# Kernel optimization log

Measured on AMD Instinct MI355X. Metric: run time of the kernel, lower is better.

## Reference

```python
import jax, jax.numpy as jnp
import numpy as np

SCALE, Z, X, Y = 4, 9, 9, 9
INV_SQRT_2PI = 1.0 / np.sqrt(2.0 * np.pi)


def setup_inputs() -> dict:
    key = jax.random.key(0)
    k1, = jax.random.split(key, 1)
    inp = jax.random.normal(k1, (1, 1, 128, 512, 512), dtype=jnp.float32)
    return {
        "inp": inp,
        "mu_z": jnp.asarray(0.0, dtype=jnp.float32),
        "sig_z": jnp.asarray(0.1, dtype=jnp.float32),
        "bet_xy": jnp.asarray(2.0, dtype=jnp.float32),
        "bet_z": jnp.asarray(1.5, dtype=jnp.float32),
    }


def _gen_alf(bet_xy, bet_z):
    # squared distances along each axis; torch's loop overwrites the wrap-around
    # write, so the net result for odd sizes is simply (arange - size//2)**2
    zd = ((jnp.arange(Z) - Z // 2) ** 2).astype(jnp.float32)[:, None, None]
    xd = ((jnp.arange(X) - X // 2) ** 2).astype(jnp.float32)[None, :, None]
    yd = ((jnp.arange(Y) - Y // 2) ** 2).astype(jnp.float32)[None, None, :]
    d_2 = zd / bet_z ** 2 + (xd + yd) / bet_xy ** 2  # (Z, X, Y)
    return jnp.exp(-d_2 / 2) * INV_SQRT_2PI


def reference(inp, mu_z, sig_z, bet_xy, bet_z):
    z0 = jnp.exp(mu_z + 0.5 * sig_z ** 2)
    rec = inp * z0  # (N, 1, D, H, W)
    alf = _gen_alf(bet_xy, bet_z)[None, None]  # (1, 1, Z, X, Y)
    pad_z = (Z - SCALE + 1) // 2
    rec = jax.lax.conv_general_dilated(
        rec, alf,
        window_strides=(SCALE, 1, 1),
        padding=[(pad_z, pad_z), (X // 2, X // 2), (Y // 2, Y // 2)],
        dimension_numbers=("NCDHW", "OIDHW", "NCDHW"),
    )  # (N, 1, D//SCALE, H, W)
    rec = (rec - rec.min()) / (rec.max() - rec.min())
    return rec
```

## Files before the change

kernel.cpp:

```cpp
#include <hip/hip_runtime.h>

#define D_IN  128
#define D_OUT 32
#define H     512
#define W     512
#define W4    128

__device__ __forceinline__ float gw(int k, float inv2) {
    float d = (float)(k - 4);
    return expf(-d * d * inv2);
}

__global__ void zconv_kernel(const float* __restrict__ inp, float* __restrict__ out,
                             const float* __restrict__ bet_z_p) {
    int tid = blockIdx.x * blockDim.x + threadIdx.x;
    int w4 = tid & (W4 - 1);
    int h  = (tid >> 7) & (H - 1);
    int d  = tid >> 16;
    float bz   = bet_z_p[0];
    float inv2 = 1.0f / (2.0f * bz * bz);
    const float4* in4 = (const float4*)inp;
    float4 acc = make_float4(0.f, 0.f, 0.f, 0.f);
    int base = h * W4 + w4;
#pragma unroll
    for (int k = 0; k < 9; ++k) {
        int din = 4 * d - 3 + k;
        if (din < 0 || din >= D_IN) continue;
        float wt = gw(k, inv2);
        float4 v = in4[din * (H * W4) + base];
        acc.x += v.x * wt; acc.y += v.y * wt; acc.z += v.z * wt; acc.w += v.w * wt;
    }
    ((float4*)out)[d * (H * W4) + base] = acc;
}

__global__ void hconv_kernel(const float* __restrict__ in, float* __restrict__ out,
                             const float* __restrict__ bet_xy_p) {
    int tid = blockIdx.x * blockDim.x + threadIdx.x;
    int w4 = tid & (W4 - 1);
    int h  = (tid >> 7) & (H - 1);
    int d  = tid >> 16;
    float b    = bet_xy_p[0];
    float inv2 = 1.0f / (2.0f * b * b);
    const float4* in4 = (const float4*)in;
    float4 acc = make_float4(0.f, 0.f, 0.f, 0.f);
#pragma unroll
    for (int k = 0; k < 9; ++k) {
        int hh = h - 4 + k;
        if (hh < 0 || hh >= H) continue;
        float wt = gw(k, inv2);
        float4 v = in4[(d * H + hh) * W4 + w4];
        acc.x += v.x * wt; acc.y += v.y * wt; acc.z += v.z * wt; acc.w += v.w * wt;
    }
    ((float4*)out)[(d * H + h) * W4 + w4] = acc;
}

__global__ void wconv_kernel(const float* __restrict__ in, float* __restrict__ out,
                             const float* __restrict__ bet_xy_p,
                             float* __restrict__ blkMin, float* __restrict__ blkMax) {
    int tid = blockIdx.x * blockDim.x + threadIdx.x;
    int w4 = tid & (W4 - 1);
    int h  = (tid >> 7) & (H - 1);
    int d  = tid >> 16;
    float b    = bet_xy_p[0];
    float inv2 = 1.0f / (2.0f * b * b);
    float wt[9];
#pragma unroll
    for (int k = 0; k < 9; ++k) wt[k] = gw(k, inv2);

    const float4* in4 = (const float4*)in;
    int row = (d * H + h) * W4;
    float4 z4 = make_float4(0.f, 0.f, 0.f, 0.f);
    float4 va = (w4 > 0)      ? in4[row + w4 - 1] : z4;
    float4 vb =                 in4[row + w4];
    float4 vc = (w4 < W4 - 1) ? in4[row + w4 + 1] : z4;
    float win[12] = {va.x, va.y, va.z, va.w,
                     vb.x, vb.y, vb.z, vb.w,
                     vc.x, vc.y, vc.z, vc.w};
    float4 o = make_float4(0.f, 0.f, 0.f, 0.f);
#pragma unroll
    for (int k = 0; k < 9; ++k) {
        o.x += win[k]     * wt[k];
        o.y += win[k + 1] * wt[k];
        o.z += win[k + 2] * wt[k];
        o.w += win[k + 3] * wt[k];
    }
    ((float4*)out)[row + w4] = o;

    float lmin = fminf(fminf(o.x, o.y), fminf(o.z, o.w));
    float lmax = fmaxf(fmaxf(o.x, o.y), fmaxf(o.z, o.w));
#pragma unroll
    for (int off = 32; off > 0; off >>= 1) {
        lmin = fminf(lmin, __shfl_down(lmin, off, 64));
        lmax = fmaxf(lmax, __shfl_down(lmax, off, 64));
    }
    __shared__ float smin[4], smax[4];
    int lane = threadIdx.x & 63, wv = threadIdx.x >> 6;
    if (lane == 0) { smin[wv] = lmin; smax[wv] = lmax; }
    __syncthreads();
    if (threadIdx.x == 0) {
        blkMin[blockIdx.x] = fminf(fminf(smin[0], smin[1]), fminf(smin[2], smin[3]));
        blkMax[blockIdx.x] = fmaxf(fmaxf(smax[0], smax[1]), fmaxf(smax[2], smax[3]));
    }
}

__global__ void reduce_kernel(const float* __restrict__ blkMin, const float* __restrict__ blkMax,
                              float* __restrict__ fin, int nblk) {
    float lmin =  3.402823466e38f;
    float lmax = -3.402823466e38f;
    for (int i = threadIdx.x; i < nblk; i += blockDim.x) {
        lmin = fminf(lmin, blkMin[i]);
        lmax = fmaxf(lmax, blkMax[i]);
    }
#pragma unroll
    for (int off = 32; off > 0; off >>= 1) {
        lmin = fminf(lmin, __shfl_down(lmin, off, 64));
        lmax = fmaxf(lmax, __shfl_down(lmax, off, 64));
    }
    __shared__ float smin[4], smax[4];
    int lane = threadIdx.x & 63, wv = threadIdx.x >> 6;
    if (lane == 0) { smin[wv] = lmin; smax[wv] = lmax; }
    __syncthreads();
    if (threadIdx.x == 0) {
        fin[0] = fminf(fminf(smin[0], smin[1]), fminf(smin[2], smin[3]));
        fin[1] = fmaxf(fmaxf(smax[0], smax[1]), fmaxf(smax[2], smax[3]));
    }
}

__global__ void norm_kernel(const float* __restrict__ in, float* __restrict__ out,
                            const float* __restrict__ fin) {
    int tid = blockIdx.x * blockDim.x + threadIdx.x;
    float mn  = fin[0];
    float inv = 1.0f / (fin[1] - mn);
    float4 v = ((const float4*)in)[tid];
    float4 o = make_float4((v.x - mn) * inv, (v.y - mn) * inv,
                           (v.z - mn) * inv, (v.w - mn) * inv);
    ((float4*)out)[tid] = o;
}

extern "C" void kernel_launch(void* const* d_in, const int* in_sizes, int n_in,
                              void* d_out, int out_size, void* d_ws, size_t ws_size,
                              hipStream_t stream) {
    const float* inp    = (const float*)d_in[0];
    const float* bet_xy = (const float*)d_in[3];
    const float* bet_z  = (const float*)d_in[4];
    float* out = (float*)d_out;

    char* ws = (char*)d_ws;
    float* fin    = (float*)ws;
    float* blkMin = (float*)(ws + 256);
    float* blkMax = (float*)(ws + 256 + 32768);
    float* bufA   = (float*)(ws + 256 + 65536);

    const int NTH  = D_OUT * H * W4;
    const int BLK  = 256;
    const int GRID = NTH / BLK;

    zconv_kernel<<<GRID, BLK, 0, stream>>>(inp, bufA, bet_z);
    hconv_kernel<<<GRID, BLK, 0, stream>>>(bufA, out, bet_xy);
    wconv_kernel<<<GRID, BLK, 0, stream>>>(out, bufA, bet_xy, blkMin, blkMax);
    reduce_kernel<<<1, BLK, 0, stream>>>(blkMin, blkMax, fin, GRID);
    norm_kernel<<<GRID, BLK, 0, stream>>>(bufA, out, fin);
}
```

Before: 275.0 us.

## Fuse z, h, w separable convolutions into one LDS-tiled kernel

Replaces the three separate z, h and w convolution kernels with a single kernel. Each block handles a 16-row strip of one output depth slice and keeps the z-convolved strip (with halo) and the h-convolved strip in shared memory. This removes two full intermediate round trips through global memory. In exchange it recomputes the z-conv for 8 halo rows per strip (24/16 of the input reads) and uses about 80KB of LDS per block, which limits occupancy.

```diff
diff --git a/kernel.cpp b/kernel.cpp
--- a/kernel.cpp
+++ b/kernel.cpp
@@ -5,101 +5,112 @@
 #define H     512
 #define W     512
 #define W4    128
+#define HB    16
+#define ZR    (HB + 8)
+#define NTHR  512
 
-__device__ __forceinline__ float gw(int k, float inv2) {
-    float d = (float)(k - 4);
-    return expf(-d * d * inv2);
-}
+__global__ __launch_bounds__(NTHR)
+void conv3d_fused(const float* __restrict__ inp, float* __restrict__ out,
+                  const float* __restrict__ bxy_p, const float* __restrict__ bz_p,
+                  float* __restrict__ blkMin, float* __restrict__ blkMax) {
+    __shared__ float zbuf[ZR * W];
+    __shared__ float hbuf[HB * W];
 
-__global__ void zconv_kernel(const float* __restrict__ inp, float* __restrict__ out,
-                             const float* __restrict__ bet_z_p) {
-    int tid = blockIdx.x * blockDim.x + threadIdx.x;
-    int w4 = tid & (W4 - 1);
-    int h  = (tid >> 7) & (H - 1);
-    int d  = tid >> 16;
-    float bz   = bet_z_p[0];
-    float inv2 = 1.0f / (2.0f * bz * bz);
-    const float4* in4 = (const float4*)inp;
-    float4 acc = make_float4(0.f, 0.f, 0.f, 0.f);
-    int base = h * W4 + w4;
+    const int d  = blockIdx.x >> 5;
+    const int h0 = (blockIdx.x & 31) * HB;
+
+    const float bz = bz_p[0], bx = bxy_p[0];
+    const float iz = 1.0f / (2.0f * bz * bz);
+    const float ix = 1.0f / (2.0f * bx * bx);
+    float wz[9], wx[9];
 #pragma unroll
     for (int k = 0; k < 9; ++k) {
-        int din = 4 * d - 3 + k;
-        if (din < 0 || din >= D_IN) continue;
-        float wt = gw(k, inv2);
-        float4 v = in4[din * (H * W4) + base];
-        acc.x += v.x * wt; acc.y += v.y * wt; acc.z += v.z * wt; acc.w += v.w * wt;
+        float dd = (float)(k - 4);
+        wz[k] = expf(-dd * dd * iz);
+        wx[k] = expf(-dd * dd * ix);
     }
-    ((float4*)out)[d * (H * W4) + base] = acc;
-}
 
-__global__ void hconv_kernel(const float* __restrict__ in, float* __restrict__ out,
-                             const float* __restrict__ bet_xy_p) {
-    int tid = blockIdx.x * blockDim.x + threadIdx.x;
-    int w4 = tid & (W4 - 1);
-    int h  = (tid >> 7) & (H - 1);
-    int d  = tid >> 16;
-    float b    = bet_xy_p[0];
-    float inv2 = 1.0f / (2.0f * b * b);
-    const float4* in4 = (const float4*)in;
-    float4 acc = make_float4(0.f, 0.f, 0.f, 0.f);
+    const float4* in4 = (const float4*)inp;
+    float4* z4 = (float4*)zbuf;
+    float4* h4 = (float4*)hbuf;
+
+    for (int t = threadIdx.x; t < ZR * W4; t += NTHR) {
+        int r  = t >> 7;
+        int c4 = t & (W4 - 1);
+        int h  = h0 - 4 + r;
+        float4 acc = make_float4(0.f, 0.f, 0.f, 0.f);
+        if ((unsigned)h < H) {
+            int base = h * W4 + c4;
 #pragma unroll
-    for (int k = 0; k < 9; ++k) {
-        int hh = h - 4 + k;
-        if (hh < 0 || hh >= H) continue;
-        float wt = gw(k, inv2);
-        float4 v = in4[(d * H + hh) * W4 + w4];
-        acc.x += v.x * wt; acc.y += v.y * wt; acc.z += v.z * wt; acc.w += v.w * wt;
+            for (int k = 0; k < 9; ++k) {
+                int din = 4 * d - 3 + k;
+                if ((unsigned)din < D_IN) {
+                    float4 v = in4[din * (H * W4) + base];
+                    acc.x += v.x * wz[k]; acc.y += v.y * wz[k];
+                    acc.z += v.z * wz[k]; acc.w += v.w * wz[k];
+                }
+            }
+        }
+        z4[t] = acc;
     }
-    ((float4*)out)[(d * H + h) * W4 + w4] = acc;
-}
+    __syncthreads();
 
-__global__ void wconv_kernel(const float* __restrict__ in, float* __restrict__ out,
-                             const float* __restrict__ bet_xy_p,
-                             float* __restrict__ blkMin, float* __restrict__ blkMax) {
-    int tid = blockIdx.x * blockDim.x + threadIdx.x;
-    int w4 = tid & (W4 - 1);
-    int h  = (tid >> 7) & (H - 1);
-    int d  = tid >> 16;
-    float b    = bet_xy_p[0];
-    float inv2 = 1.0f / (2.0f * b * b);
-    float wt[9];
+    for (int t = threadIdx.x; t < HB * W4; t += NTHR) {
+        int r  = t >> 7;
+        int c4 = t & (W4 - 1);
+        float4 acc = make_float4(0.f, 0.f, 0.f, 0.f);
 #pragma unroll
-    for (int k = 0; k < 9; ++k) wt[k] = gw(k, inv2);
+        for (int k = 0; k < 9; ++k) {
+            float4 v = z4[(r + k) * W4 + c4];
+            acc.x += v.x * wx[k]; acc.y += v.y * wx[k];
+            acc.z += v.z * wx[k]; acc.w += v.w * wx[k];
+        }
+        h4[t] = acc;
+    }
+    __syncthreads();
 
-    const float4* in4 = (const float4*)in;
-    int row = (d * H + h) * W4;
-    float4 z4 = make_float4(0.f, 0.f, 0.f, 0.f);
-    float4 va = (w4 > 0)      ? in4[row + w4 - 1] : z4;
-    float4 vb =                 in4[row + w4];
-    float4 vc = (w4 < W4 - 1) ? in4[row + w4 + 1] : z4;
-    float win[12] = {va.x, va.y, va.z, va.w,
-                     vb.x, vb.y, vb.z, vb.w,
-                     vc.x, vc.y, vc.z, vc.w};
-    float4 o = make_float4(0.f, 0.f, 0.f, 0.f);
+    float lmin =  3.402823466e38f;
+    float lmax = -3.402823466e38f;
+    float4* out4 = (float4*)out;
+    for (int t = threadIdx.x; t < HB * W4; t += NTHR) {
+        int r  = t >> 7;
+        int c4 = t & (W4 - 1);
+        float4 zv = make_float4(0.f, 0.f, 0.f, 0.f);
+        float4 va = (c4 > 0)      ? h4[r * W4 + c4 - 1] : zv;
+        float4 vb =                 h4[r * W4 + c4];
+        float4 vc = (c4 < W4 - 1) ? h4[r * W4 + c4 + 1] : zv;
+        float win[12] = {va.x, va.y, va.z, va.w,
+                         vb.x, vb.y, vb.z, vb.w,
+                         vc.x, vc.y, vc.z, vc.w};
+        float4 o = make_float4(0.f, 0.f, 0.f, 0.f);
 #pragma unroll
-    for (int k = 0; k < 9; ++k) {
-        o.x += win[k]     * wt[k];
-        o.y += win[k + 1] * wt[k];
-        o.z += win[k + 2] * wt[k];
-        o.w += win[k + 3] * wt[k];
+        for (int k = 0; k < 9; ++k) {
+            o.x += win[k]     * wx[k];
+            o.y += win[k + 1] * wx[k];
+            o.z += win[k + 2] * wx[k];
+            o.w += win[k + 3] * wx[k];
+        }
+        out4[(d * H + h0 + r) * W4 + c4] = o;
+        lmin = fminf(lmin, fminf(fminf(o.x, o.y), fminf(o.z, o.w)));
+        lmax = fmaxf(lmax, fmaxf(fmaxf(o.x, o.y), fmaxf(o.z, o.w)));
     }
-    ((float4*)out)[row + w4] = o;
 
-    float lmin = fminf(fminf(o.x, o.y), fminf(o.z, o.w));
-    float lmax = fmaxf(fmaxf(o.x, o.y), fmaxf(o.z, o.w));
 #pragma unroll
     for (int off = 32; off > 0; off >>= 1) {
         lmin = fminf(lmin, __shfl_down(lmin, off, 64));
         lmax = fmaxf(lmax, __shfl_down(lmax, off, 64));
     }
-    __shared__ float smin[4], smax[4];
+    float* smin = &zbuf[0];
+    float* smax = &zbuf[16];
     int lane = threadIdx.x & 63, wv = threadIdx.x >> 6;
     if (lane == 0) { smin[wv] = lmin; smax[wv] = lmax; }
     __syncthreads();
     if (threadIdx.x == 0) {
-        blkMin[blockIdx.x] = fminf(fminf(smin[0], smin[1]), fminf(smin[2], smin[3]));
-        blkMax[blockIdx.x] = fmaxf(fmaxf(smax[0], smax[1]), fmaxf(smax[2], smax[3]));
+        float mn = smin[0], mx = smax[0];
+#pragma unroll
+        for (int i = 1; i < 8; ++i) { mn = fminf(mn, smin[i]); mx = fmaxf(mx, smax[i]); }
+        blkMin[blockIdx.x] = mn;
+        blkMax[blockIdx.x] = mx;
     }
 }
 
@@ -132,9 +143,8 @@
     float mn  = fin[0];
     float inv = 1.0f / (fin[1] - mn);
     float4 v = ((const float4*)in)[tid];
-    float4 o = make_float4((v.x - mn) * inv, (v.y - mn) * inv,
-                           (v.z - mn) * inv, (v.w - mn) * inv);
-    ((float4*)out)[tid] = o;
+    ((float4*)out)[tid] = make_float4((v.x - mn) * inv, (v.y - mn) * inv,
+                                      (v.z - mn) * inv, (v.w - mn) * inv);
 }
 
 extern "C" void kernel_launch(void* const* d_in, const int* in_sizes, int n_in,
@@ -147,17 +157,14 @@
 
     char* ws = (char*)d_ws;
     float* fin    = (float*)ws;
-    float* blkMin = (float*)(ws + 256);
-    float* blkMax = (float*)(ws + 256 + 32768);
-    float* bufA   = (float*)(ws + 256 + 65536);
+    float* blkMin = (float*)(ws + 4096);
+    float* blkMax = (float*)(ws + 8192);
+    float* bufA   = (float*)(ws + 65536);
 
-    const int NTH  = D_OUT * H * W4;
-    const int BLK  = 256;
-    const int GRID = NTH / BLK;
+    const int CONV_GRID = D_OUT * (H / HB);
+    conv3d_fused<<<CONV_GRID, NTHR, 0, stream>>>(inp, bufA, bet_xy, bet_z, blkMin, blkMax);
+    reduce_kernel<<<1, 256, 0, stream>>>(blkMin, blkMax, fin, CONV_GRID);
 
-    zconv_kernel<<<GRID, BLK, 0, stream>>>(inp, bufA, bet_z);
-    hconv_kernel<<<GRID, BLK, 0, stream>>>(bufA, out, bet_xy);
-    wconv_kernel<<<GRID, BLK, 0, stream>>>(out, bufA, bet_xy, blkMin, blkMax);
-    reduce_kernel<<<1, BLK, 0, stream>>>(blkMin, blkMax, fin, GRID);
-    norm_kernel<<<GRID, BLK, 0, stream>>>(bufA, out, fin);
+    const int NTASK = D_OUT * H * W4;
+    norm_kernel<<<NTASK / 256, 256, 0, stream>>>(bufA, out, fin);
 }
```

After: 242.3 us. 1.14x faster.
